# Kernel tuning notes

Hardware: AMD Instinct MI355X
Metric: run time of the kernel (lower is better)

Reference implementation:

```python
import math
import jax, jax.numpy as jnp
import numpy as np

B, H, N, D = 2, 16, 8192, 64
NUM_PROJS = 7
BLOCK = 256      # key/query block size
SAMPLE = 256     # sample_size


def _gray_perm(num_projs):
    # AngularLSH._unit_hamming_distance_array: gray-code ordering of 2**num_projs buckets
    a = np.array([0, 1], dtype=np.int32)
    for i in range(1, num_projs):
        a = np.concatenate([a, a[::-1] + 2 ** i])
    return a


def _lsh_hash(mat, pd, perm, enc):
    # mat: [B,H,N,D], pd: [D,R] -> bucket id per position, gray-code permuted
    mask = jnp.einsum('bhnd,dr->bhnr', mat, pd) > 0
    bin_ids = (mask.astype(jnp.int32) * enc).sum(-1)
    return perm[bin_ids]


def _exact_attention(q, k, v, scale, bias=None):
    # q: [...,n,d], k/v: [...,m,d]
    s = jnp.einsum('...nd,...md->...nm', q, k) * scale
    if bias is not None:
        s = s + bias
    lse = jax.scipy.special.logsumexp(s, axis=-1, keepdims=True)
    attn = jnp.einsum('...nm,...md->...nd', jnp.exp(s - lse), v)
    return attn, lse


def _add_self_attentions(a1, l1, a2, l2):
    c = jax.nn.sigmoid(l1 - l2)          # 1 / (1 + exp(l2 - l1))
    attn = c * a1 + (1.0 - c) * a2
    lse = jnp.logaddexp(l1, l2)
    return attn, lse


def setup_inputs() -> dict:
    key = jax.random.key(0)
    kq, kk, kv, kp, ks = jax.random.split(key, 5)
    return {
        'query': jax.random.normal(kq, (B, H, N, D), dtype=jnp.float32),
        'key': jax.random.normal(kk, (B, H, N, D), dtype=jnp.float32),
        'value': jax.random.normal(kv, (B, H, N, D), dtype=jnp.float32),
        'proj_dir': jax.random.normal(kp, (1, 1, D, NUM_PROJS), dtype=jnp.float32),
        'sampled_set': jax.random.randint(ks, (B, H, SAMPLE), 0, N, dtype=jnp.int32),
    }


def reference(query, key, value, proj_dir, sampled_set):
    scale = D ** -0.5
    pd = proj_dir[0, 0]                                  # [D, R]
    perm = jnp.asarray(_gray_perm(NUM_PROJS))
    enc = 2 ** jnp.arange(NUM_PROJS, dtype=jnp.int32)

    gather = lambda x, idx: jnp.take_along_axis(x, idx[..., None], axis=2)

    # --- LSH hash + stable sort of queries/keys into buckets ---
    q_hash = _lsh_hash(query, pd, perm, enc)
    k_hash = _lsh_hash(key, pd, perm, enc)
    q_sort_idx = jnp.argsort(q_hash, axis=2, stable=True)
    k_sort_idx = jnp.argsort(k_hash, axis=2, stable=True)
    q_sort_idx_inv = jnp.argsort(q_sort_idx, axis=2, stable=True)

    q_sorted = gather(query, q_sort_idx)
    k_sorted = gather(key, k_sort_idx)
    v_sorted = gather(value, k_sort_idx)

    # --- block-diagonal exact attention over sorted order ---
    num_blocks = N // BLOCK
    qb = q_sorted.reshape(B, H, num_blocks, BLOCK, D)
    kb = k_sorted.reshape(B, H, num_blocks, BLOCK, D)
    vb = v_sorted.reshape(B, H, num_blocks, BLOCK, D)
    attn_block, lse_block = _exact_attention(qb, kb, vb, scale)
    attn_block = attn_block.reshape(B, H, N, D)
    lse_block = lse_block.reshape(B, H, N, 1)

    # --- uniform sampling fallback (residual estimate), masking block collisions ---
    k_sub = gather(k_sorted, sampled_set)                # [B,H,SAMPLE,D]
    v_sub = gather(v_sorted, sampled_set)
    offset_blk = (jnp.arange(N) // BLOCK)[None, None, :, None]     # [1,1,N,1]
    sample_blk = (sampled_set // BLOCK)[:, :, None, :]             # [B,H,1,SAMPLE]
    collide = offset_blk == sample_blk                             # [B,H,N,SAMPLE]
    bias = jnp.where(collide, jnp.finfo(q_sorted.dtype).min, 0.0).astype(q_sorted.dtype)
    attn_res, lse_res = _exact_attention(q_sorted, k_sub, v_sub, scale, bias)
    lse_res = lse_res + math.log(N / SAMPLE)             # importance weight

    # --- online-softmax style merge, then un-sort queries ---
    attn, lse = _add_self_attentions(attn_block, lse_block, attn_res, lse_res)
    attn = gather(attn, q_sort_idx_inv)
    return attn
```

## Files before the change

kernel.cpp:

```cpp
#include <hip/hip_runtime.h>
#include <hip/hip_bf16.h>
#include <math.h>

#define B_ 2
#define H_ 16
#define N_ 8192
#define D_ 64
#define R_ 7
#define BLOCK_ 256
#define SAMPLE_ 256
#define BH_ (B_*H_)
#define NBLK_ (N_/BLOCK_)

#define CHUNK_ 128
#define PADK 72
#define PADV 132

typedef __attribute__((ext_vector_type(8))) short bf16x8;
typedef __attribute__((ext_vector_type(4))) short bf16x4;
typedef __attribute__((ext_vector_type(4))) float f32x4;
typedef __attribute__((ext_vector_type(2))) unsigned int u32x2;
typedef __attribute__((ext_vector_type(4))) unsigned int u32x4;

__device__ inline unsigned short f2bf(float x) {
  __hip_bfloat16 h = __float2bfloat16(x);
  return *(unsigned short*)&h;
}
__device__ inline unsigned int pack2bf(float a, float b) {
  return (unsigned int)f2bf(a) | ((unsigned int)f2bf(b) << 16);
}
__device__ inline float fexp2(float x) {
#if __has_builtin(__builtin_amdgcn_exp2f)
  return __builtin_amdgcn_exp2f(x);
#else
  return exp2f(x);
#endif
}

__device__ inline f32x4 mfma16(bf16x4 a, bf16x4 b, f32x4 c) {
#if __has_builtin(__builtin_amdgcn_mfma_f32_16x16x16bf16_1k)
  return __builtin_amdgcn_mfma_f32_16x16x16bf16_1k(a, b, c, 0, 0, 0);
#else
  asm volatile("v_mfma_f32_16x16x16_bf16 %0, %1, %2, %0" : "+v"(c) : "v"(a), "v"(b));
  return c;
#endif
}

__global__ __launch_bounds__(256) void hash_kernel(
    const float* __restrict__ q, const float* __restrict__ k,
    const float* __restrict__ pd, int* __restrict__ qh, int* __restrict__ kh) {
  __shared__ __align__(16) float spdT[R_][D_];
  for (int i = threadIdx.x; i < D_ * R_; i += blockDim.x) {
    int d = i / R_, r = i - d * R_;
    spdT[r][d] = pd[i];
  }
  __syncthreads();
  int tid = blockIdx.x * blockDim.x + threadIdx.x;
  const int half = BH_ * N_;
  const float* src = (tid < half) ? q : k;
  int* dst = (tid < half) ? qh : kh;
  int row = (tid < half) ? tid : tid - half;
  const float4* x4 = (const float4*)(src + (size_t)row * D_);
  float4 x[16];
#pragma unroll
  for (int j = 0; j < 16; j++) x[j] = x4[j];
  int bin = 0;
#pragma unroll
  for (int r = 0; r < R_; r++) {
    float a = 0.f;
#pragma unroll
    for (int j = 0; j < 16; j++) {
      float4 sp = *(const float4*)&spdT[r][4 * j];
      a = fmaf(x[j].x, sp.x, a);
      a = fmaf(x[j].y, sp.y, a);
      a = fmaf(x[j].z, sp.z, a);
      a = fmaf(x[j].w, sp.w, a);
    }
    bin |= (a > 0.f) ? (1 << r) : 0;
  }
  dst[row] = bin ^ (bin >> 1);
}

__global__ __launch_bounds__(256) void sort_kernel(
    const int* __restrict__ qh, const int* __restrict__ kh,
    int* __restrict__ qidx, int* __restrict__ kidx) {
  int g = blockIdx.x;
  int bh = g & (BH_ - 1);
  bool isK = g >= BH_;
  const int* h = (isK ? kh : qh) + (size_t)bh * N_;
  int* idx = (isK ? kidx : qidx) + (size_t)bh * N_;
  __shared__ unsigned short hist[128][256];
  __shared__ int segsum[128][8];
  __shared__ int tot[128];
  __shared__ int off[128];
  const int t = threadIdx.x;

  {
    u32x4* hz = (u32x4*)hist;
    for (int i = t; i < 4096; i += 256) hz[i] = (u32x4){0u, 0u, 0u, 0u};
  }
  __syncthreads();

  const int base = t * 32;
  int hv[32];
#pragma unroll
  for (int j = 0; j < 32; j++) hv[j] = h[base + j];
#pragma unroll
  for (int j = 0; j < 32; j++) hist[hv[j]][t]++;
  __syncthreads();

  for (int task = t; task < 1024; task += 256) {
    int b = task >> 3, s = task & 7;
    int sum = 0;
#pragma unroll
    for (int u = 0; u < 32; u++) sum += hist[b][s * 32 + u];
    segsum[b][s] = sum;
  }
  __syncthreads();

  if (t < 128) {
    int run = 0;
#pragma unroll
    for (int s = 0; s < 8; s++) { int x = segsum[t][s]; segsum[t][s] = run; run += x; }
    tot[t] = run;
  }
  __syncthreads();

  if (t == 0) {
    int run = 0;
    for (int b = 0; b < 128; b++) { off[b] = run; run += tot[b]; }
  }
  __syncthreads();

  for (int task = t; task < 1024; task += 256) {
    int b = task >> 3, s = task & 7;
    int run = off[b] + segsum[b][s];
#pragma unroll
    for (int u = 0; u < 32; u++) {
      int x = hist[b][s * 32 + u];
      hist[b][s * 32 + u] = (unsigned short)run;
      run += x;
    }
  }
  __syncthreads();

#pragma unroll
  for (int j = 0; j < 32; j++) {
    int c = hv[j];
    int p = hist[c][t]++;
    idx[p] = base + j;
  }
}

__global__ __launch_bounds__(256) void subgather_kernel(
    const float* __restrict__ key, const float* __restrict__ val,
    const int* __restrict__ kidx, const int* __restrict__ samp,
    float* __restrict__ ksub, float* __restrict__ vsub, int* __restrict__ sblk) {
  int sidx = blockIdx.x * 4 + (threadIdx.x >> 6);
  int bh = sidx >> 8;
  int d = threadIdx.x & 63;
  int pos = samp[sidx];
  int row = kidx[(size_t)bh * N_ + pos];
  ksub[(size_t)sidx * D_ + d] = key[((size_t)bh * N_ + row) * D_ + d];
  vsub[(size_t)sidx * D_ + d] = val[((size_t)bh * N_ + row) * D_ + d];
  if (d == 0) sblk[sidx] = pos >> 8;
}

__global__ __launch_bounds__(512, 4) void attn_kernel(
    const float* __restrict__ query, const float* __restrict__ key,
    const float* __restrict__ value,
    const int* __restrict__ qidx, const int* __restrict__ kidx,
    const float* __restrict__ ksub, const float* __restrict__ vsub,
    const int* __restrict__ sblk, float* __restrict__ out) {
  __shared__ __align__(16) unsigned short KsL[CHUNK_ * PADK];
  __shared__ __align__(16) unsigned short VtL[D_ * PADV];
  __shared__ int sbs[CHUNK_];
  __shared__ int qrows[BLOCK_];

  const int bh = blockIdx.x / NBLK_;
  const int blk = blockIdx.x - bh * NBLK_;
  const int tid = threadIdx.x;
  const int w = tid >> 6;
  const int lane = tid & 63;
  const int lg = lane >> 4;
  const int lr = lane & 15;
  const float FOLD = 0.18033688011112042f;

  const int kp = tid >> 3, dq = tid & 7;
  auto stage_kv = [&](const float* kr0, const float* kr1,
                      const float* vr0, const float* vr1, int kbase) {
    float4 ka0 = *(const float4*)(kr0), ka1 = *(const float4*)(kr0 + 4);
    float4 kb0 = *(const float4*)(kr1), kb1 = *(const float4*)(kr1 + 4);
    u32x4 pk0 = (u32x4){pack2bf(ka0.x, ka0.y), pack2bf(ka0.z, ka0.w),
                        pack2bf(ka1.x, ka1.y), pack2bf(ka1.z, ka1.w)};
    u32x4 pk1 = (u32x4){pack2bf(kb0.x, kb0.y), pack2bf(kb0.z, kb0.w),
                        pack2bf(kb1.x, kb1.y), pack2bf(kb1.z, kb1.w)};
    *(u32x4*)&KsL[(kbase + 0) * PADK + dq * 8] = pk0;
    *(u32x4*)&KsL[(kbase + 1) * PADK + dq * 8] = pk1;
    float4 va0 = *(const float4*)(vr0), va1 = *(const float4*)(vr0 + 4);
    float4 vb0 = *(const float4*)(vr1), vb1 = *(const float4*)(vr1 + 4);
    float a[8] = {va0.x, va0.y, va0.z, va0.w, va1.x, va1.y, va1.z, va1.w};
    float b[8] = {vb0.x, vb0.y, vb0.z, vb0.w, vb1.x, vb1.y, vb1.z, vb1.w};
#pragma unroll
    for (int j = 0; j < 8; j++)
      *(unsigned*)&VtL[(dq * 8 + j) * PADV + kbase] = pack2bf(a[j], b[j]);
  };
  auto stage_block = [&](int c) {
    size_t ib = (size_t)bh * N_ + blk * BLOCK_ + c * CHUNK_ + 2 * kp;
    int r0 = kidx[ib], r1 = kidx[ib + 1];
    const float* k0 = key + ((size_t)bh * N_ + r0) * D_ + dq * 8;
    const float* k1 = key + ((size_t)bh * N_ + r1) * D_ + dq * 8;
    const float* v0 = value + ((size_t)bh * N_ + r0) * D_ + dq * 8;
    const float* v1 = value + ((size_t)bh * N_ + r1) * D_ + dq * 8;
    stage_kv(k0, k1, v0, v1, 2 * kp);
  };
  auto stage_sample = [&](int c) {
    size_t b0 = ((size_t)bh * SAMPLE_ + c * CHUNK_ + 2 * kp) * D_ + dq * 8;
    stage_kv(ksub + b0, ksub + b0 + D_, vsub + b0, vsub + b0 + D_, 2 * kp);
    if (tid < CHUNK_) sbs[tid] = sblk[(size_t)bh * SAMPLE_ + c * CHUNK_ + tid];
  };

  stage_block(0);
  if (tid < BLOCK_) qrows[tid] = qidx[(size_t)bh * N_ + blk * BLOCK_ + tid];
  __syncthreads();

  bf16x8 qf[2][2];
#pragma unroll
  for (int qt = 0; qt < 2; qt++) {
    int qrow = qrows[w * 32 + qt * 16 + lr];
    const float* qp = query + ((size_t)bh * N_ + qrow) * D_ + lg * 8;
#pragma unroll
    for (int h = 0; h < 2; h++) {
      float4 a = *(const float4*)(qp + h * 32);
      float4 b = *(const float4*)(qp + h * 32 + 4);
      union { u32x4 u; bf16x8 v; } cv;
      cv.u = (u32x4){pack2bf(a.x * FOLD, a.y * FOLD), pack2bf(a.z * FOLD, a.w * FOLD),
                     pack2bf(b.x * FOLD, b.y * FOLD), pack2bf(b.z * FOLD, b.w * FOLD)};
      qf[qt][h] = cv.v;
    }
  }

  f32x4 oA[2][4], oB[2][4];
  float lsA[2] = {0.f, 0.f}, lsB[2] = {0.f, 0.f};
#pragma unroll
  for (int a = 0; a < 2; a++)
#pragma unroll
    for (int b = 0; b < 4; b++) { oA[a][b] = (f32x4){0.f,0.f,0.f,0.f}; oB[a][b] = (f32x4){0.f,0.f,0.f,0.f}; }

  auto phase = [&](f32x4 (&o)[2][4], float (&ls)[2], bool masked) {
#pragma unroll 2
    for (int kt = 0; kt < 8; kt++) {
      const unsigned short* krow = &KsL[(kt * 16 + lr) * PADK + lg * 8];
      bf16x8 ak0 = *(const bf16x8*)(krow);
      bf16x8 ak1 = *(const bf16x8*)(krow + 32);
      bf16x4 av[4];
#pragma unroll
      for (int dt = 0; dt < 4; dt++)
        av[dt] = *(const bf16x4*)(&VtL[(dt * 16 + lr) * PADV + kt * 16 + lg * 4]);
      float msk[4];
      if (masked) {
#pragma unroll
        for (int r = 0; r < 4; r++)
          msk[r] = (sbs[kt * 16 + lg * 4 + r] == blk) ? 0.f : 1.f;
      }
      bf16x4 bq[2];
#pragma unroll
      for (int qt = 0; qt < 2; qt++) {
        f32x4 c = (f32x4){0.f, 0.f, 0.f, 0.f};
        c = __builtin_amdgcn_mfma_f32_16x16x32_bf16(ak0, qf[qt][0], c, 0, 0, 0);
        c = __builtin_amdgcn_mfma_f32_16x16x32_bf16(ak1, qf[qt][1], c, 0, 0, 0);
        float w0 = fexp2(c[0]), w1 = fexp2(c[1]);
        float w2 = fexp2(c[2]), w3 = fexp2(c[3]);
        if (masked) { w0 *= msk[0]; w1 *= msk[1]; w2 *= msk[2]; w3 *= msk[3]; }
        ls[qt] += (w0 + w1) + (w2 + w3);
        union { u32x2 u; bf16x4 v; } cv;
        cv.u = (u32x2){pack2bf(w0, w1), pack2bf(w2, w3)};
        bq[qt] = cv.v;
      }
#pragma unroll
      for (int qt = 0; qt < 2; qt++)
#pragma unroll
        for (int dt = 0; dt < 4; dt++)
          o[qt][dt] = mfma16(av[dt], bq[qt], o[qt][dt]);
    }
  };

  phase(oA, lsA, false);
  __syncthreads();
  stage_block(1);
  __syncthreads();
  phase(oA, lsA, false);
  __syncthreads();

  stage_sample(0);
  __syncthreads();
  phase(oB, lsB, true);
  __syncthreads();
  stage_sample(1);
  __syncthreads();
  phase(oB, lsB, true);

#pragma unroll
  for (int qt = 0; qt < 2; qt++) {
    float lb = lsA[qt];
    lb += __shfl_xor(lb, 16); lb += __shfl_xor(lb, 32);
    float lrv = lsB[qt];
    lrv += __shfl_xor(lrv, 16); lrv += __shfl_xor(lrv, 32);
    float wb, wr;
    float lseb = __logf(lb);
    if (lrv > 0.f) {
      float lser = __logf(lrv) + 3.4657359027997265f;
      float cc = 1.f / (1.f + __expf(lser - lseb));
      wb = cc / lb; wr = (1.f - cc) / lrv;
    } else {
      wb = 1.f / lb; wr = 0.f;
    }
    int qr = qrows[w * 32 + qt * 16 + lr];
    float* op = out + ((size_t)bh * N_ + qr) * D_ + lg * 4;
#pragma unroll
    for (int dt = 0; dt < 4; dt++) {
      float4 o;
      o.x = wb * oA[qt][dt][0] + wr * oB[qt][dt][0];
      o.y = wb * oA[qt][dt][1] + wr * oB[qt][dt][1];
      o.z = wb * oA[qt][dt][2] + wr * oB[qt][dt][2];
      o.w = wb * oA[qt][dt][3] + wr * oB[qt][dt][3];
      *(float4*)(op + dt * 16) = o;
    }
  }
}

extern "C" void kernel_launch(void* const* d_in, const int* in_sizes, int n_in,
                              void* d_out, int out_size, void* d_ws, size_t ws_size,
                              hipStream_t stream) {
  const float* query = (const float*)d_in[0];
  const float* key   = (const float*)d_in[1];
  const float* value = (const float*)d_in[2];
  const float* pd    = (const float*)d_in[3];
  const int*   samp  = (const int*)d_in[4];
  float* out = (float*)d_out;

  char* w = (char*)d_ws;
  size_t o = 0;
  auto alloc = [&](size_t bytes) { void* p = w + o; o = (o + bytes + 255) & ~(size_t)255; return p; };
  int* qh   = (int*)alloc((size_t)BH_ * N_ * 4);
  int* kh   = (int*)alloc((size_t)BH_ * N_ * 4);
  int* qidx = (int*)alloc((size_t)BH_ * N_ * 4);
  int* kidx = (int*)alloc((size_t)BH_ * N_ * 4);
  float* ksub = (float*)alloc((size_t)BH_ * SAMPLE_ * D_ * 4);
  float* vsub = (float*)alloc((size_t)BH_ * SAMPLE_ * D_ * 4);
  int* sblk = (int*)alloc((size_t)BH_ * SAMPLE_ * 4);

  hash_kernel<<<(2 * BH_ * N_) / 256, 256, 0, stream>>>(query, key, pd, qh, kh);
  sort_kernel<<<2 * BH_, 256, 0, stream>>>(qh, kh, qidx, kidx);
  subgather_kernel<<<BH_ * SAMPLE_ / 4, 256, 0, stream>>>(key, value, kidx, samp, ksub, vsub, sblk);
  attn_kernel<<<BH_ * NBLK_, 512, 0, stream>>>(query, key, value, qidx, kidx,
                                               ksub, vsub, sblk, out);
}
```

Measured before the change: 119.8 us.

## Prefetch next K/V chunk into registers while computing the current chunk

Splits the shared-memory staging into a global load into registers and a later write to LDS, so the next chunk's gather is issued before the current compute phase and its latency is hidden. Query row indices are loaded directly per lane instead of through an LDS array, which removes one barrier. The minimum blocks per CU in launch bounds drops from 4 to 3 to make room for the extra prefetch registers, at the cost of possible lower occupancy.

```diff
diff --git a/kernel.cpp b/kernel.cpp
--- a/kernel.cpp
+++ b/kernel.cpp
@@ -166,7 +166,7 @@
   if (d == 0) sblk[sidx] = pos >> 8;
 }
 
-__global__ __launch_bounds__(512, 4) void attn_kernel(
+__global__ __launch_bounds__(512, 3) void attn_kernel(
     const float* __restrict__ query, const float* __restrict__ key,
     const float* __restrict__ value,
     const int* __restrict__ qidx, const int* __restrict__ kidx,
@@ -175,7 +175,6 @@
   __shared__ __align__(16) unsigned short KsL[CHUNK_ * PADK];
   __shared__ __align__(16) unsigned short VtL[D_ * PADV];
   __shared__ int sbs[CHUNK_];
-  __shared__ int qrows[BLOCK_];
 
   const int bh = blockIdx.x / NBLK_;
   const int blk = blockIdx.x - bh * NBLK_;
@@ -185,60 +184,73 @@
   const int lg = lane >> 4;
   const int lr = lane & 15;
   const float FOLD = 0.18033688011112042f;
-
   const int kp = tid >> 3, dq = tid & 7;
-  auto stage_kv = [&](const float* kr0, const float* kr1,
-                      const float* vr0, const float* vr1, int kbase) {
-    float4 ka0 = *(const float4*)(kr0), ka1 = *(const float4*)(kr0 + 4);
-    float4 kb0 = *(const float4*)(kr1), kb1 = *(const float4*)(kr1 + 4);
-    u32x4 pk0 = (u32x4){pack2bf(ka0.x, ka0.y), pack2bf(ka0.z, ka0.w),
-                        pack2bf(ka1.x, ka1.y), pack2bf(ka1.z, ka1.w)};
-    u32x4 pk1 = (u32x4){pack2bf(kb0.x, kb0.y), pack2bf(kb0.z, kb0.w),
-                        pack2bf(kb1.x, kb1.y), pack2bf(kb1.z, kb1.w)};
-    *(u32x4*)&KsL[(kbase + 0) * PADK + dq * 8] = pk0;
-    *(u32x4*)&KsL[(kbase + 1) * PADK + dq * 8] = pk1;
-    float4 va0 = *(const float4*)(vr0), va1 = *(const float4*)(vr0 + 4);
-    float4 vb0 = *(const float4*)(vr1), vb1 = *(const float4*)(vr1 + 4);
-    float a[8] = {va0.x, va0.y, va0.z, va0.w, va1.x, va1.y, va1.z, va1.w};
-    float b[8] = {vb0.x, vb0.y, vb0.z, vb0.w, vb1.x, vb1.y, vb1.z, vb1.w};
-#pragma unroll
-    for (int j = 0; j < 8; j++)
-      *(unsigned*)&VtL[(dq * 8 + j) * PADV + kbase] = pack2bf(a[j], b[j]);
-  };
-  auto stage_block = [&](int c) {
+
+  float4 sk0a, sk0b, sk1a, sk1b, sv0a, sv0b, sv1a, sv1b;
+  int sreg = 0;
+
+  auto load_block = [&](int c) {
     size_t ib = (size_t)bh * N_ + blk * BLOCK_ + c * CHUNK_ + 2 * kp;
     int r0 = kidx[ib], r1 = kidx[ib + 1];
     const float* k0 = key + ((size_t)bh * N_ + r0) * D_ + dq * 8;
     const float* k1 = key + ((size_t)bh * N_ + r1) * D_ + dq * 8;
     const float* v0 = value + ((size_t)bh * N_ + r0) * D_ + dq * 8;
     const float* v1 = value + ((size_t)bh * N_ + r1) * D_ + dq * 8;
-    stage_kv(k0, k1, v0, v1, 2 * kp);
+    sk0a = *(const float4*)k0; sk0b = *(const float4*)(k0 + 4);
+    sk1a = *(const float4*)k1; sk1b = *(const float4*)(k1 + 4);
+    sv0a = *(const float4*)v0; sv0b = *(const float4*)(v0 + 4);
+    sv1a = *(const float4*)v1; sv1b = *(const float4*)(v1 + 4);
   };
-  auto stage_sample = [&](int c) {
+  auto load_sample = [&](int c) {
     size_t b0 = ((size_t)bh * SAMPLE_ + c * CHUNK_ + 2 * kp) * D_ + dq * 8;
-    stage_kv(ksub + b0, ksub + b0 + D_, vsub + b0, vsub + b0 + D_, 2 * kp);
-    if (tid < CHUNK_) sbs[tid] = sblk[(size_t)bh * SAMPLE_ + c * CHUNK_ + tid];
+    sk0a = *(const float4*)(ksub + b0);      sk0b = *(const float4*)(ksub + b0 + 4);
+    sk1a = *(const float4*)(ksub + b0 + D_); sk1b = *(const float4*)(ksub + b0 + D_ + 4);
+    sv0a = *(const float4*)(vsub + b0);      sv0b = *(const float4*)(vsub + b0 + 4);
+    sv1a = *(const float4*)(vsub + b0 + D_); sv1b = *(const float4*)(vsub + b0 + D_ + 4);
+    if (tid < CHUNK_) sreg = sblk[(size_t)bh * SAMPLE_ + c * CHUNK_ + tid];
   };
-
-  stage_block(0);
-  if (tid < BLOCK_) qrows[tid] = qidx[(size_t)bh * N_ + blk * BLOCK_ + tid];
-  __syncthreads();
-
+  auto write_kv = [&](bool issb) {
+    u32x4 pk0 = (u32x4){pack2bf(sk0a.x, sk0a.y), pack2bf(sk0a.z, sk0a.w),
+                        pack2bf(sk0b.x, sk0b.y), pack2bf(sk0b.z, sk0b.w)};
+    u32x4 pk1 = (u32x4){pack2bf(sk1a.x, sk1a.y), pack2bf(sk1a.z, sk1a.w),
+                        pack2bf(sk1b.x, sk1b.y), pack2bf(sk1b.z, sk1b.w)};
+    *(u32x4*)&KsL[(2 * kp + 0) * PADK + dq * 8] = pk0;
+    *(u32x4*)&KsL[(2 * kp + 1) * PADK + dq * 8] = pk1;
+    float a0[8] = {sv0a.x, sv0a.y, sv0a.z, sv0a.w, sv0b.x, sv0b.y, sv0b.z, sv0b.w};
+    float a1[8] = {sv1a.x, sv1a.y, sv1a.z, sv1a.w, sv1b.x, sv1b.y, sv1b.z, sv1b.w};
+#pragma unroll
+    for (int j = 0; j < 8; j++)
+      *(unsigned*)&VtL[(dq * 8 + j) * PADV + 2 * kp] = pack2bf(a0[j], a1[j]);
+    if (issb && tid < CHUNK_) sbs[tid] = sreg;
+  };
+
+  load_block(0);
+  int qrw[2];
+  qrw[0] = qidx[(size_t)bh * N_ + blk * BLOCK_ + w * 32 + lr];
+  qrw[1] = qidx[(size_t)bh * N_ + blk * BLOCK_ + w * 32 + 16 + lr];
+  float4 qraw[2][4];
+#pragma unroll
+  for (int qt = 0; qt < 2; qt++) {
+    const float* qp = query + ((size_t)bh * N_ + qrw[qt]) * D_ + lg * 8;
+    qraw[qt][0] = *(const float4*)(qp);
+    qraw[qt][1] = *(const float4*)(qp + 4);
+    qraw[qt][2] = *(const float4*)(qp + 32);
+    qraw[qt][3] = *(const float4*)(qp + 36);
+  }
+  write_kv(false);
   bf16x8 qf[2][2];
 #pragma unroll
   for (int qt = 0; qt < 2; qt++) {
-    int qrow = qrows[w * 32 + qt * 16 + lr];
-    const float* qp = query + ((size_t)bh * N_ + qrow) * D_ + lg * 8;
 #pragma unroll
     for (int h = 0; h < 2; h++) {
-      float4 a = *(const float4*)(qp + h * 32);
-      float4 b = *(const float4*)(qp + h * 32 + 4);
+      float4 a = qraw[qt][2 * h], b = qraw[qt][2 * h + 1];
       union { u32x4 u; bf16x8 v; } cv;
       cv.u = (u32x4){pack2bf(a.x * FOLD, a.y * FOLD), pack2bf(a.z * FOLD, a.w * FOLD),
                      pack2bf(b.x * FOLD, b.y * FOLD), pack2bf(b.z * FOLD, b.w * FOLD)};
       qf[qt][h] = cv.v;
     }
   }
+  __syncthreads();
 
   f32x4 oA[2][4], oB[2][4];
   float lsA[2] = {0.f, 0.f}, lsB[2] = {0.f, 0.f};
@@ -285,19 +297,24 @@
     }
   };
 
+  load_block(1);
   phase(oA, lsA, false);
   __syncthreads();
-  stage_block(1);
-  __syncthreads();
+  write_kv(false);
+  __syncthreads();
+
+  load_sample(0);
   phase(oA, lsA, false);
   __syncthreads();
-
-  stage_sample(0);
-  __syncthreads();
+  write_kv(true);
+  __syncthreads();
+
+  load_sample(1);
   phase(oB, lsB, true);
   __syncthreads();
-  stage_sample(1);
-  __syncthreads();
+  write_kv(true);
+  __syncthreads();
+
   phase(oB, lsB, true);
 
 #pragma unroll
@@ -315,8 +332,7 @@
     } else {
       wb = 1.f / lb; wr = 0.f;
     }
-    int qr = qrows[w * 32 + qt * 16 + lr];
-    float* op = out + ((size_t)bh * N_ + qr) * D_ + lg * 4;
+    float* op = out + ((size_t)bh * N_ + qrw[qt]) * D_ + lg * 4;
 #pragma unroll
     for (int dt = 0; dt < 4; dt++) {
       float4 o;
```

After: 135.7 us. 1.13x slower.

## Fuse sample gather into key sort kernel and raise MFMA phase priority

Applied to the files above, without the earlier changes.

Removes the separate subgather launch. The key-sort workgroups now gather the sampled key/value rows and block ids right after the scatter, reading the just-written kidx through global memory after a barrier. This saves one kernel launch and its dependency gap. In exchange the gather runs on only 32 workgroups, which serialises work that used to be spread across 2048 blocks. The attention phase loop is also wrapped in s_setprio(1)/s_setprio(0) so MFMA-heavy waves get scheduling priority over waves that are staging data.

```diff
diff --git a/kernel.cpp b/kernel.cpp
--- a/kernel.cpp
+++ b/kernel.cpp
@@ -83,7 +83,10 @@
 
 __global__ __launch_bounds__(256) void sort_kernel(
     const int* __restrict__ qh, const int* __restrict__ kh,
-    int* __restrict__ qidx, int* __restrict__ kidx) {
+    int* __restrict__ qidx, int* __restrict__ kidx,
+    const float* __restrict__ key, const float* __restrict__ val,
+    const int* __restrict__ samp,
+    float* __restrict__ ksub, float* __restrict__ vsub, int* __restrict__ sblk) {
   int g = blockIdx.x;
   int bh = g & (BH_ - 1);
   bool isK = g >= BH_;
@@ -150,20 +153,23 @@
     int p = hist[c][t]++;
     idx[p] = base + j;
   }
-}
-
-__global__ __launch_bounds__(256) void subgather_kernel(
-    const float* __restrict__ key, const float* __restrict__ val,
-    const int* __restrict__ kidx, const int* __restrict__ samp,
-    float* __restrict__ ksub, float* __restrict__ vsub, int* __restrict__ sblk) {
-  int sidx = blockIdx.x * 4 + (threadIdx.x >> 6);
-  int bh = sidx >> 8;
-  int d = threadIdx.x & 63;
-  int pos = samp[sidx];
-  int row = kidx[(size_t)bh * N_ + pos];
-  ksub[(size_t)sidx * D_ + d] = key[((size_t)bh * N_ + row) * D_ + d];
-  vsub[(size_t)sidx * D_ + d] = val[((size_t)bh * N_ + row) * D_ + d];
-  if (d == 0) sblk[sidx] = pos >> 8;
+
+  if (isK) {
+    __syncthreads();
+    int* srows = (int*)hist;
+    int pos = samp[(size_t)bh * SAMPLE_ + t];
+    int row = idx[pos];
+    srows[t] = row;
+    sblk[(size_t)bh * SAMPLE_ + t] = pos >> 8;
+    __syncthreads();
+    const int d = t & 63;
+    for (int it = 0; it < 64; it++) {
+      int s = it * 4 + (t >> 6);
+      int r = srows[s];
+      ksub[((size_t)bh * SAMPLE_ + s) * D_ + d] = key[((size_t)bh * N_ + r) * D_ + d];
+      vsub[((size_t)bh * SAMPLE_ + s) * D_ + d] = val[((size_t)bh * N_ + r) * D_ + d];
+    }
+  }
 }
 
 __global__ __launch_bounds__(512, 4) void attn_kernel(
@@ -248,6 +254,7 @@
     for (int b = 0; b < 4; b++) { oA[a][b] = (f32x4){0.f,0.f,0.f,0.f}; oB[a][b] = (f32x4){0.f,0.f,0.f,0.f}; }
 
   auto phase = [&](f32x4 (&o)[2][4], float (&ls)[2], bool masked) {
+    __builtin_amdgcn_s_setprio(1);
 #pragma unroll 2
     for (int kt = 0; kt < 8; kt++) {
       const unsigned short* krow = &KsL[(kt * 16 + lr) * PADK + lg * 8];
@@ -283,6 +290,7 @@
         for (int dt = 0; dt < 4; dt++)
           o[qt][dt] = mfma16(av[dt], bq[qt], o[qt][dt]);
     }
+    __builtin_amdgcn_s_setprio(0);
   };
 
   phase(oA, lsA, false);
@@ -351,8 +359,8 @@
   int* sblk = (int*)alloc((size_t)BH_ * SAMPLE_ * 4);
 
   hash_kernel<<<(2 * BH_ * N_) / 256, 256, 0, stream>>>(query, key, pd, qh, kh);
-  sort_kernel<<<2 * BH_, 256, 0, stream>>>(qh, kh, qidx, kidx);
-  subgather_kernel<<<BH_ * SAMPLE_ / 4, 256, 0, stream>>>(key, value, kidx, samp, ksub, vsub, sblk);
+  sort_kernel<<<2 * BH_, 256, 0, stream>>>(qh, kh, qidx, kidx,
+                                           key, value, samp, ksub, vsub, sblk);
   attn_kernel<<<BH_ * NBLK_, 512, 0, stream>>>(query, key, value, qidx, kidx,
                                                ksub, vsub, sblk, out);
 }
```

New measurement: 126.5 us. 1.06x slower.
